# Kernel tuning notes

Hardware: AMD Instinct MI355X
Metric: run time of the kernel (lower is better)

## Reference

```python
import jax, jax.numpy as jnp
import numpy as np

B, D, H, STEPS = 32768, 8, 64, 100


def setup_inputs() -> dict:
    key = jax.random.key(0)
    ks = jax.random.split(key, 7)
    def lin(k, shape, fan_in):
        # torch nn.Linear default init: U(-1/sqrt(fan_in), 1/sqrt(fan_in))
        return jax.random.uniform(k, shape, jnp.float32, -1.0, 1.0) / np.sqrt(fan_in).astype(np.float32)
    return {
        "x0": jax.random.normal(ks[0], (B, D), jnp.float32),
        "W1": lin(ks[1], (H, D + 1), D + 1),
        "b1": lin(ks[2], (H,), D + 1),
        "W2": lin(ks[3], (H, H), H),
        "b2": lin(ks[4], (H,), H),
        "W3": lin(ks[5], (D, H), H),
        "b3": lin(ks[6], (D,), H),
        "num_steps": STEPS,
    }


def _mlp(x, t_col, W1, b1, W2, b2, W3, b3):
    # x: [B, D], t_col: [B, 1] -> dx/dt: [B, D]
    xt = jnp.concatenate([x, t_col], axis=1)          # [B, D+1]
    h = jnp.tanh(xt @ W1.T + b1)                      # [B, H]
    h = jnp.tanh(h @ W2.T + b2)                       # [B, H]
    return h @ W3.T + b3                              # [B, D]


def reference(x0, W1, b1, W2, b2, W3, b3, num_steps):
    t0, t1 = 0.0, 1.0
    dt = (t1 - t0) / num_steps
    n, d = x0.shape
    ones_out = jnp.ones((n, d), x0.dtype)

    def step(carry, i):
        x, ld = carry
        t_col = jnp.full((n, 1), t0, x0.dtype) + i.astype(x0.dtype) * dt
        dx = _mlp(x, t_col, W1, b1, W2, b2, W3, b3)
        x_new = x + dt * dx
        # Faithful to torch source: grad of dx_dt.sum() wrt x evaluated at the
        # POST-step x (this is J^T @ 1, then summed over input dims).
        f = lambda xx: _mlp(xx, t_col, W1, b1, W2, b2, W3, b3)
        _, vjp_fn = jax.vjp(f, x_new)
        (g,) = vjp_fn(ones_out)                       # [B, D]
        ld_new = ld + dt * g.sum(axis=1)
        return (x_new, ld_new), None

    init = (x0, jnp.zeros(n, x0.dtype))
    (x, log_det), _ = jax.lax.scan(step, init, jnp.arange(num_steps))
    return x, log_det
```

## Files before the change

### kernel.cpp

```cpp
#include <hip/hip_runtime.h>


#define TSCALE 2.885390081777926815f

__device__ __forceinline__ float ftanh_s(float z) {
    float e = __builtin_amdgcn_exp2f(z);
    float r = __builtin_amdgcn_rcpf(e + 1.0f);
    return fmaf(-2.0f, r, 1.0f);
}

typedef __attribute__((ext_vector_type(8))) _Float16 v8h;
typedef __attribute__((ext_vector_type(2))) __fp16 v2fp;
typedef __attribute__((ext_vector_type(4))) float v4f;
typedef __attribute__((ext_vector_type(2))) float v2f;

union FragU {
    v8h h;
    unsigned u[4];
};

__device__ __forceinline__ unsigned pk16(float a, float b) {
    v2fp t = __builtin_amdgcn_cvt_pkrtz(a, b);
    return __builtin_bit_cast(unsigned, t);
}
__device__ __forceinline__ unsigned pk16v(v2f v) { return pk16(v.x, v.y); }

__device__ __forceinline__ int physj(int ks, int q, int jj) {
    return 16 * (ks + 2 * (jj >> 2)) + 4 * q + (jj & 3);
}

__device__ __forceinline__ void rename(const uint2 ph[4], FragU bh[2]) {
#pragma unroll
    for (int ks = 0; ks < 2; ++ks) {
        bh[ks].u[0] = ph[ks].x;
        bh[ks].u[1] = ph[ks].y;
        bh[ks].u[2] = ph[ks + 2].x;
        bh[ks].u[3] = ph[ks + 2].y;
    }
}

__global__ __launch_bounds__(256, 2) void cnf_fused(
    const float* __restrict__ x0, const float* __restrict__ W1,
    const float* __restrict__ b1, const float* __restrict__ W2,
    const float* __restrict__ b2, const float* __restrict__ W3,
    const float* __restrict__ b3, const int* __restrict__ nsp,
    float* __restrict__ out, int rows) {
    const int tid = threadIdx.x;
    const int w = tid >> 6;
    const int lane = tid & 63;
    const int c = lane & 15;
    const int q = lane >> 4;
    const int row0 = blockIdx.x * 64 + w * 16;

    const int n = *nsp;
    const float dt = 1.0f / (float)n;

    FragU a1[4];
#pragma unroll
    for (int mt = 0; mt < 4; ++mt) {
        const int m = 16 * mt + c;
        float f[8] = {0.f, 0.f, 0.f, 0.f, 0.f, 0.f, 0.f, 0.f};
        if (q == 0) {
#pragma unroll
            for (int jj = 0; jj < 4; ++jj) f[jj] = TSCALE * W1[m * 9 + jj];
            f[4] = TSCALE * W1[m * 9 + 8];
            f[5] = TSCALE * b1[m];
        } else if (q == 1) {
#pragma unroll
            for (int jj = 0; jj < 4; ++jj) f[jj] = TSCALE * W1[m * 9 + 4 + jj];
        }
#pragma unroll
        for (int p = 0; p < 4; ++p) a1[mt].u[p] = pk16(f[2 * p], f[2 * p + 1]);
    }
    FragU a2[4][2], a2g[4][2], a2d[4][2];
#pragma unroll
    for (int mt = 0; mt < 4; ++mt) {
        const int m = 16 * mt + c;
        float w3cm = 0.f;
#pragma unroll
        for (int d = 0; d < 8; ++d) w3cm += W3[d * 64 + m];
#pragma unroll
        for (int ks = 0; ks < 2; ++ks) {
            float f[8], fg[8], fd[8];
#pragma unroll
            for (int jj = 0; jj < 8; ++jj) {
                const int pj = physj(ks, q, jj);
                const float wv = W2[m * 64 + pj];
                float w1r = 0.f;
#pragma unroll
                for (int k = 0; k < 8; ++k) w1r += W1[pj * 9 + k];
                f[jj] = TSCALE * wv;
                fg[jj] = w3cm * wv * w1r;
                fd[jj] = wv * (dt * W1[pj * 9 + 8]);
            }
#pragma unroll
            for (int p = 0; p < 4; ++p) {
                a2[mt][ks].u[p] = pk16(f[2 * p], f[2 * p + 1]);
                a2g[mt][ks].u[p] = pk16(fg[2 * p], fg[2 * p + 1]);
                a2d[mt][ks].u[p] = pk16(fd[2 * p], fd[2 * p + 1]);
            }
        }
    }
    FragU a3[2];
#pragma unroll
    for (int ks = 0; ks < 2; ++ks) {
        float f[8];
#pragma unroll
        for (int jj = 0; jj < 8; ++jj) f[jj] = W3[(c & 7) * 64 + physj(ks, q, jj)];
#pragma unroll
        for (int p = 0; p < 4; ++p) a3[ks].u[p] = pk16(f[2 * p], f[2 * p + 1]);
    }
    v4f vb2[4];
#pragma unroll
    for (int mt = 0; mt < 4; ++mt) {
        const int j0 = 16 * mt + 4 * q;
        vb2[mt][0] = TSCALE * b2[j0]; vb2[mt][1] = TSCALE * b2[j0 + 1];
        vb2[mt][2] = TSCALE * b2[j0 + 2]; vb2[mt][3] = TSCALE * b2[j0 + 3];
    }
    v4f vb3;
#pragma unroll
    for (int r = 0; r < 4; ++r) vb3[r] = b3[(4 * q + r) & 7];

    float xr[4];
    {
        float4 v = *(const float4*)(x0 + (size_t)(row0 + c) * 8 + 4 * (q & 1));
        xr[0] = v.x; xr[1] = v.y; xr[2] = v.z; xr[3] = v.w;
    }
    const v4f vzero = {0.f, 0.f, 0.f, 0.f};
    v2f gv = {0.f, 0.f};

    {
        FragU bx;
        bx.u[0] = pk16(xr[0], xr[1]);
        bx.u[1] = pk16(xr[2], xr[3]);
        bx.u[2] = pk16(0.0f, 1.0f);
        bx.u[3] = 0u;
        v4f d1[4];
#pragma unroll
        for (int mt = 0; mt < 4; ++mt)
            d1[mt] = __builtin_amdgcn_mfma_f32_16x16x32_f16(a1[mt].h, bx.h, vzero, 0, 0, 0);
        uint2 ph[4];
#pragma unroll
        for (int mt = 0; mt < 4; ++mt) {
            ph[mt].x = pk16(ftanh_s(d1[mt][0]), ftanh_s(d1[mt][1]));
            ph[mt].y = pk16(ftanh_s(d1[mt][2]), ftanh_s(d1[mt][3]));
        }
        FragU bh[2];
        rename(ph, bh);
        v4f d2[4];
#pragma unroll
        for (int mt = 0; mt < 4; ++mt) {
            d2[mt] = __builtin_amdgcn_mfma_f32_16x16x32_f16(a2[mt][0].h, bh[0].h, vb2[mt], 0, 0, 0);
            d2[mt] = __builtin_amdgcn_mfma_f32_16x16x32_f16(a2[mt][1].h, bh[1].h, d2[mt], 0, 0, 0);
        }
#pragma unroll
        for (int mt = 0; mt < 4; ++mt) {
            ph[mt].x = pk16(ftanh_s(d2[mt][0]), ftanh_s(d2[mt][1]));
            ph[mt].y = pk16(ftanh_s(d2[mt][2]), ftanh_s(d2[mt][3]));
        }
        FragU bh2[2];
        rename(ph, bh2);
        v4f d3;
        d3 = __builtin_amdgcn_mfma_f32_16x16x32_f16(a3[0].h, bh2[0].h, vb3, 0, 0, 0);
        d3 = __builtin_amdgcn_mfma_f32_16x16x32_f16(a3[1].h, bh2[1].h, d3, 0, 0, 0);
#pragma unroll
        for (int r = 0; r < 4; ++r) xr[r] = fmaf(dt, d3[r], xr[r]);
    }

    float tp = 0.0f;
    for (int i = 1; i < n; ++i) {
        FragU bx;
        bx.u[0] = pk16(xr[0], xr[1]);
        bx.u[1] = pk16(xr[2], xr[3]);
        bx.u[2] = pk16(tp, 1.0f);
        bx.u[3] = 0u;
        tp += dt;
        v4f d1[4];
#pragma unroll
        for (int mt = 0; mt < 4; ++mt)
            d1[mt] = __builtin_amdgcn_mfma_f32_16x16x32_f16(a1[mt].h, bx.h, vzero, 0, 0, 0);

        uint2 phb[4], pom[4];
#pragma unroll
        for (int mt = 0; mt < 4; ++mt) {
            v2f th01 = {ftanh_s(d1[mt][0]), ftanh_s(d1[mt][1])};
            v2f th23 = {ftanh_s(d1[mt][2]), ftanh_s(d1[mt][3])};
            v2f om01 = v2f{1.f, 1.f} - th01 * th01;
            v2f om23 = v2f{1.f, 1.f} - th23 * th23;
            phb[mt].x = pk16v(th01);
            phb[mt].y = pk16v(th23);
            pom[mt].x = pk16v(om01);
            pom[mt].y = pk16v(om23);
        }
        FragU bhb[2], bo[2];
        rename(phb, bhb);
        rename(pom, bo);

        v4f z2b[4], sg[4], dz2[4];
#pragma unroll
        for (int mt = 0; mt < 4; ++mt) {
            z2b[mt] = __builtin_amdgcn_mfma_f32_16x16x32_f16(a2[mt][0].h, bhb[0].h, vb2[mt], 0, 0, 0);
            z2b[mt] = __builtin_amdgcn_mfma_f32_16x16x32_f16(a2[mt][1].h, bhb[1].h, z2b[mt], 0, 0, 0);
            sg[mt] = __builtin_amdgcn_mfma_f32_16x16x32_f16(a2g[mt][0].h, bo[0].h, vzero, 0, 0, 0);
            sg[mt] = __builtin_amdgcn_mfma_f32_16x16x32_f16(a2g[mt][1].h, bo[1].h, sg[mt], 0, 0, 0);
            dz2[mt] = __builtin_amdgcn_mfma_f32_16x16x32_f16(a2d[mt][0].h, bo[0].h, vzero, 0, 0, 0);
            dz2[mt] = __builtin_amdgcn_mfma_f32_16x16x32_f16(a2d[mt][1].h, bo[1].h, dz2[mt], 0, 0, 0);
        }

        uint2 ph2[4];
#pragma unroll
        for (int mt = 0; mt < 4; ++mt) {
            v2f th01 = {ftanh_s(z2b[mt][0]), ftanh_s(z2b[mt][1])};
            v2f th23 = {ftanh_s(z2b[mt][2]), ftanh_s(z2b[mt][3])};
            v2f om01 = v2f{1.f, 1.f} - th01 * th01;
            v2f om23 = v2f{1.f, 1.f} - th23 * th23;
            gv += om01 * v2f{sg[mt][0], sg[mt][1]};
            gv += om23 * v2f{sg[mt][2], sg[mt][3]};
            v2f tf01 = om01 * v2f{dz2[mt][0], dz2[mt][1]} + th01;
            v2f tf23 = om23 * v2f{dz2[mt][2], dz2[mt][3]} + th23;
            ph2[mt].x = pk16v(tf01);
            ph2[mt].y = pk16v(tf23);
        }
        FragU bh2[2];
        rename(ph2, bh2);
        v4f d3;
        d3 = __builtin_amdgcn_mfma_f32_16x16x32_f16(a3[0].h, bh2[0].h, vb3, 0, 0, 0);
        d3 = __builtin_amdgcn_mfma_f32_16x16x32_f16(a3[1].h, bh2[1].h, d3, 0, 0, 0);
#pragma unroll
        for (int r = 0; r < 4; ++r) xr[r] = fmaf(dt, d3[r], xr[r]);
    }

    {
        FragU bx;
        bx.u[0] = pk16(xr[0], xr[1]);
        bx.u[1] = pk16(xr[2], xr[3]);
        bx.u[2] = pk16(tp, 1.0f);
        bx.u[3] = 0u;
        v4f d1[4];
#pragma unroll
        for (int mt = 0; mt < 4; ++mt)
            d1[mt] = __builtin_amdgcn_mfma_f32_16x16x32_f16(a1[mt].h, bx.h, vzero, 0, 0, 0);
        uint2 phb[4], pom[4];
#pragma unroll
        for (int mt = 0; mt < 4; ++mt) {
            v2f th01 = {ftanh_s(d1[mt][0]), ftanh_s(d1[mt][1])};
            v2f th23 = {ftanh_s(d1[mt][2]), ftanh_s(d1[mt][3])};
            v2f om01 = v2f{1.f, 1.f} - th01 * th01;
            v2f om23 = v2f{1.f, 1.f} - th23 * th23;
            phb[mt].x = pk16v(th01);
            phb[mt].y = pk16v(th23);
            pom[mt].x = pk16v(om01);
            pom[mt].y = pk16v(om23);
        }
        FragU bhb[2], bo[2];
        rename(phb, bhb);
        rename(pom, bo);
        v4f z2b[4], sg[4];
#pragma unroll
        for (int mt = 0; mt < 4; ++mt) {
            z2b[mt] = __builtin_amdgcn_mfma_f32_16x16x32_f16(a2[mt][0].h, bhb[0].h, vb2[mt], 0, 0, 0);
            z2b[mt] = __builtin_amdgcn_mfma_f32_16x16x32_f16(a2[mt][1].h, bhb[1].h, z2b[mt], 0, 0, 0);
            sg[mt] = __builtin_amdgcn_mfma_f32_16x16x32_f16(a2g[mt][0].h, bo[0].h, vzero, 0, 0, 0);
            sg[mt] = __builtin_amdgcn_mfma_f32_16x16x32_f16(a2g[mt][1].h, bo[1].h, sg[mt], 0, 0, 0);
        }
#pragma unroll
        for (int mt = 0; mt < 4; ++mt) {
            v2f th01 = {ftanh_s(z2b[mt][0]), ftanh_s(z2b[mt][1])};
            v2f th23 = {ftanh_s(z2b[mt][2]), ftanh_s(z2b[mt][3])};
            v2f om01 = v2f{1.f, 1.f} - th01 * th01;
            v2f om23 = v2f{1.f, 1.f} - th23 * th23;
            gv += om01 * v2f{sg[mt][0], sg[mt][1]};
            gv += om23 * v2f{sg[mt][2], sg[mt][3]};
        }
    }

    float g = gv.x + gv.y;
    g += __shfl_xor(g, 16);
    g += __shfl_xor(g, 32);
    if (q < 2) {
        float4 st = {xr[0], xr[1], xr[2], xr[3]};
        *(float4*)(out + (size_t)(row0 + c) * 8 + 4 * q) = st;
    }
    if (q == 0) out[(size_t)rows * 8 + row0 + c] = dt * g;
}

extern "C" void kernel_launch(void* const* d_in, const int* in_sizes, int n_in,
                              void* d_out, int out_size, void* d_ws, size_t ws_size,
                              hipStream_t stream) {
    const float* x0 = (const float*)d_in[0];
    const float* W1 = (const float*)d_in[1];
    const float* b1 = (const float*)d_in[2];
    const float* W2 = (const float*)d_in[3];
    const float* b2 = (const float*)d_in[4];
    const float* W3 = (const float*)d_in[5];
    const float* b3 = (const float*)d_in[6];
    const int* ns = (const int*)d_in[7];
    float* out = (float*)d_out;
    const int rows = in_sizes[0] / 8;

    hipLaunchKernelGGL(cnf_fused, dim3(rows / 64), dim3(256), 0, stream,
                       x0, W1, b1, W2, b2, W3, b3, ns, out, rows);
}
```

Measured before the change: 202.9 us.

## Fold scaled W2 variants into B-operand scaling to drop extra weight fragments

Drops the two extra precomputed W2-derived A fragments (a2g, a2d) and reuses the single TSCALE-scaled a2 fragment for all three layer-2 MFMA chains. The per-column factors (W1 row sums, dt*W1 time column) are applied to the B operand with packed fp16 multiplies, and the per-row W3 column sum is applied afterwards in fp32. This cuts register pressure by dozens of VGPRs per lane, which may help scheduling or occupancy, at the cost of a few packed multiplies per step and some extra fp16 rounding.

```diff
diff --git a/kernel.cpp b/kernel.cpp
--- a/kernel.cpp
+++ b/kernel.cpp
@@ -24,6 +24,13 @@
     return __builtin_bit_cast(unsigned, t);
 }
 __device__ __forceinline__ unsigned pk16v(v2f v) { return pk16(v.x, v.y); }
+
+__device__ __forceinline__ unsigned pmul16(unsigned a, unsigned b) {
+    v2fp x = __builtin_bit_cast(v2fp, a);
+    v2fp y = __builtin_bit_cast(v2fp, b);
+    v2fp r = x * y;
+    return __builtin_bit_cast(unsigned, r);
+}
 
 __device__ __forceinline__ int physj(int ks, int q, int jj) {
     return 16 * (ks + 2 * (jj >> 2)) + 4 * q + (jj & 3);
@@ -54,6 +61,7 @@
 
     const int n = *nsp;
     const float dt = 1.0f / (float)n;
+    const float inv_ts = 1.0f / TSCALE;
 
     FragU a1[4];
 #pragma unroll
@@ -72,33 +80,44 @@
 #pragma unroll
         for (int p = 0; p < 4; ++p) a1[mt].u[p] = pk16(f[2 * p], f[2 * p + 1]);
     }
-    FragU a2[4][2], a2g[4][2], a2d[4][2];
+    FragU a2[4][2];
 #pragma unroll
     for (int mt = 0; mt < 4; ++mt) {
-        const int m = 16 * mt + c;
-        float w3cm = 0.f;
-#pragma unroll
-        for (int d = 0; d < 8; ++d) w3cm += W3[d * 64 + m];
 #pragma unroll
         for (int ks = 0; ks < 2; ++ks) {
-            float f[8], fg[8], fd[8];
-#pragma unroll
-            for (int jj = 0; jj < 8; ++jj) {
-                const int pj = physj(ks, q, jj);
-                const float wv = W2[m * 64 + pj];
-                float w1r = 0.f;
-#pragma unroll
-                for (int k = 0; k < 8; ++k) w1r += W1[pj * 9 + k];
-                f[jj] = TSCALE * wv;
-                fg[jj] = w3cm * wv * w1r;
-                fd[jj] = wv * (dt * W1[pj * 9 + 8]);
+            float f[8];
+#pragma unroll
+            for (int jj = 0; jj < 8; ++jj)
+                f[jj] = TSCALE * W2[(16 * mt + c) * 64 + physj(ks, q, jj)];
+#pragma unroll
+            for (int p = 0; p < 4; ++p) a2[mt][ks].u[p] = pk16(f[2 * p], f[2 * p + 1]);
+        }
+    }
+    unsigned cpk[4][2], w1rpk[4][2];
+    v4f w3cf[4];
+#pragma unroll
+    for (int mt = 0; mt < 4; ++mt) {
+#pragma unroll
+        for (int p = 0; p < 2; ++p) {
+            const int j0 = 16 * mt + 4 * q + 2 * p;
+            const float c0 = dt * inv_ts * W1[j0 * 9 + 8];
+            const float c1 = dt * inv_ts * W1[(j0 + 1) * 9 + 8];
+            cpk[mt][p] = pk16(c0, c1);
+            float r0 = 0.f, r1 = 0.f;
+#pragma unroll
+            for (int k = 0; k < 8; ++k) {
+                r0 += W1[j0 * 9 + k];
+                r1 += W1[(j0 + 1) * 9 + k];
             }
-#pragma unroll
-            for (int p = 0; p < 4; ++p) {
-                a2[mt][ks].u[p] = pk16(f[2 * p], f[2 * p + 1]);
-                a2g[mt][ks].u[p] = pk16(fg[2 * p], fg[2 * p + 1]);
-                a2d[mt][ks].u[p] = pk16(fd[2 * p], fd[2 * p + 1]);
-            }
+            w1rpk[mt][p] = pk16(r0, r1);
+        }
+#pragma unroll
+        for (int r = 0; r < 4; ++r) {
+            const int h = 16 * mt + 4 * q + r;
+            float s = 0.f;
+#pragma unroll
+            for (int d = 0; d < 8; ++d) s += W3[d * 64 + h];
+            w3cf[mt][r] = s * inv_ts;
         }
     }
     FragU a3[2];
@@ -192,19 +211,28 @@
             pom[mt].x = pk16v(om01);
             pom[mt].y = pk16v(om23);
         }
-        FragU bhb[2], bo[2];
+        uint2 pb2[4], pb3[4];
+#pragma unroll
+        for (int mt = 0; mt < 4; ++mt) {
+            pb2[mt].x = pmul16(pom[mt].x, cpk[mt][0]);
+            pb2[mt].y = pmul16(pom[mt].y, cpk[mt][1]);
+            pb3[mt].x = pmul16(pom[mt].x, w1rpk[mt][0]);
+            pb3[mt].y = pmul16(pom[mt].y, w1rpk[mt][1]);
+        }
+        FragU bhb[2], bo2f[2], bo3f[2];
         rename(phb, bhb);
-        rename(pom, bo);
+        rename(pb2, bo2f);
+        rename(pb3, bo3f);
 
         v4f z2b[4], sg[4], dz2[4];
 #pragma unroll
         for (int mt = 0; mt < 4; ++mt) {
             z2b[mt] = __builtin_amdgcn_mfma_f32_16x16x32_f16(a2[mt][0].h, bhb[0].h, vb2[mt], 0, 0, 0);
             z2b[mt] = __builtin_amdgcn_mfma_f32_16x16x32_f16(a2[mt][1].h, bhb[1].h, z2b[mt], 0, 0, 0);
-            sg[mt] = __builtin_amdgcn_mfma_f32_16x16x32_f16(a2g[mt][0].h, bo[0].h, vzero, 0, 0, 0);
-            sg[mt] = __builtin_amdgcn_mfma_f32_16x16x32_f16(a2g[mt][1].h, bo[1].h, sg[mt], 0, 0, 0);
-            dz2[mt] = __builtin_amdgcn_mfma_f32_16x16x32_f16(a2d[mt][0].h, bo[0].h, vzero, 0, 0, 0);
-            dz2[mt] = __builtin_amdgcn_mfma_f32_16x16x32_f16(a2d[mt][1].h, bo[1].h, dz2[mt], 0, 0, 0);
+            sg[mt] = __builtin_amdgcn_mfma_f32_16x16x32_f16(a2[mt][0].h, bo3f[0].h, vzero, 0, 0, 0);
+            sg[mt] = __builtin_amdgcn_mfma_f32_16x16x32_f16(a2[mt][1].h, bo3f[1].h, sg[mt], 0, 0, 0);
+            dz2[mt] = __builtin_amdgcn_mfma_f32_16x16x32_f16(a2[mt][0].h, bo2f[0].h, vzero, 0, 0, 0);
+            dz2[mt] = __builtin_amdgcn_mfma_f32_16x16x32_f16(a2[mt][1].h, bo2f[1].h, dz2[mt], 0, 0, 0);
         }
 
         uint2 ph2[4];
@@ -214,8 +242,8 @@
             v2f th23 = {ftanh_s(z2b[mt][2]), ftanh_s(z2b[mt][3])};
             v2f om01 = v2f{1.f, 1.f} - th01 * th01;
             v2f om23 = v2f{1.f, 1.f} - th23 * th23;
-            gv += om01 * v2f{sg[mt][0], sg[mt][1]};
-            gv += om23 * v2f{sg[mt][2], sg[mt][3]};
+            gv += om01 * (v2f{w3cf[mt][0], w3cf[mt][1]} * v2f{sg[mt][0], sg[mt][1]});
+            gv += om23 * (v2f{w3cf[mt][2], w3cf[mt][3]} * v2f{sg[mt][2], sg[mt][3]});
             v2f tf01 = om01 * v2f{dz2[mt][0], dz2[mt][1]} + th01;
             v2f tf23 = om23 * v2f{dz2[mt][2], dz2[mt][3]} + th23;
             ph2[mt].x = pk16v(tf01);
@@ -252,16 +280,22 @@
             pom[mt].x = pk16v(om01);
             pom[mt].y = pk16v(om23);
         }
-        FragU bhb[2], bo[2];
+        uint2 pb3[4];
+#pragma unroll
+        for (int mt = 0; mt < 4; ++mt) {
+            pb3[mt].x = pmul16(pom[mt].x, w1rpk[mt][0]);
+            pb3[mt].y = pmul16(pom[mt].y, w1rpk[mt][1]);
+        }
+        FragU bhb[2], bo3f[2];
         rename(phb, bhb);
-        rename(pom, bo);
+        rename(pb3, bo3f);
         v4f z2b[4], sg[4];
 #pragma unroll
         for (int mt = 0; mt < 4; ++mt) {
             z2b[mt] = __builtin_amdgcn_mfma_f32_16x16x32_f16(a2[mt][0].h, bhb[0].h, vb2[mt], 0, 0, 0);
             z2b[mt] = __builtin_amdgcn_mfma_f32_16x16x32_f16(a2[mt][1].h, bhb[1].h, z2b[mt], 0, 0, 0);
-            sg[mt] = __builtin_amdgcn_mfma_f32_16x16x32_f16(a2g[mt][0].h, bo[0].h, vzero, 0, 0, 0);
-            sg[mt] = __builtin_amdgcn_mfma_f32_16x16x32_f16(a2g[mt][1].h, bo[1].h, sg[mt], 0, 0, 0);
+            sg[mt] = __builtin_amdgcn_mfma_f32_16x16x32_f16(a2[mt][0].h, bo3f[0].h, vzero, 0, 0, 0);
+            sg[mt] = __builtin_amdgcn_mfma_f32_16x16x32_f16(a2[mt][1].h, bo3f[1].h, sg[mt], 0, 0, 0);
         }
 #pragma unroll
         for (int mt = 0; mt < 4; ++mt) {
@@ -269,8 +303,8 @@
             v2f th23 = {ftanh_s(z2b[mt][2]), ftanh_s(z2b[mt][3])};
             v2f om01 = v2f{1.f, 1.f} - th01 * th01;
             v2f om23 = v2f{1.f, 1.f} - th23 * th23;
-            gv += om01 * v2f{sg[mt][0], sg[mt][1]};
-            gv += om23 * v2f{sg[mt][2], sg[mt][3]};
+            gv += om01 * (v2f{w3cf[mt][0], w3cf[mt][1]} * v2f{sg[mt][0], sg[mt][1]});
+            gv += om23 * (v2f{w3cf[mt][2], w3cf[mt][3]} * v2f{sg[mt][2], sg[mt][3]});
         }
     }
 
```

After: 206.6 us. No clear change (+1.8%).
